# Optimization experiments

Hardware: AMD Instinct MI355X
Metric: run time of the kernel (lower is better)

Reference implementation:

```python
import jax, jax.numpy as jnp
import numpy as np

D_MODEL = 2048
EXP_RATE = 4
DEPTH = 1
EPS = 1e-5

def setup_inputs() -> dict:
    key = jax.random.key(0)
    k1, k2 = jax.random.split(key, 2)
    B, T, D, E = 4, 4096, D_MODEL, EXP_RATE
    x = jax.random.normal(k1, (B, T, D), dtype=jnp.float32)
    residual = jax.random.normal(k2, (B, T, D), dtype=jnp.float32)
    # static_alpha = cat([alpha0, eye(E)], dim=1) -> [E, E+1]
    alpha0 = np.zeros((E, 1), dtype=np.float32)
    alpha0[DEPTH % E, 0] = 1.0
    static_alpha = jnp.asarray(np.concatenate([alpha0, np.eye(E, dtype=np.float32)], axis=1))
    static_beta = jnp.ones((E,), dtype=jnp.float32)
    dynamic_alpha_fn = jnp.zeros((D, E + 1), dtype=jnp.float32)
    dynamic_alpha_scale = jnp.ones((1,), dtype=jnp.float32) * 0.01
    dynamic_beta_fn = jnp.zeros((D,), dtype=jnp.float32)
    dynamic_beta_scale = jnp.ones((1,), dtype=jnp.float32) * 0.01
    rms_weight = jnp.ones((D,), dtype=jnp.float32)
    return {
        "x": x, "residual": residual, "rms_weight": rms_weight,
        "static_alpha": static_alpha, "static_beta": static_beta,
        "dynamic_alpha_fn": dynamic_alpha_fn, "dynamic_alpha_scale": dynamic_alpha_scale,
        "dynamic_beta_fn": dynamic_beta_fn, "dynamic_beta_scale": dynamic_beta_scale,
    }

def reference(x, residual, rms_weight, static_alpha, static_beta,
              dynamic_alpha_fn, dynamic_alpha_scale, dynamic_beta_fn, dynamic_beta_scale):
    # RMSNorm (elementwise affine)
    norm_x = x * jax.lax.rsqrt(jnp.mean(x * x, axis=-1, keepdims=True) + EPS) * rms_weight
    # Dynamic params
    dyn_alpha = jnp.tanh(norm_x @ dynamic_alpha_fn) * dynamic_alpha_scale  # [B,T,E+1]
    dyn_beta = jnp.tanh(norm_x @ dynamic_beta_fn) * dynamic_beta_scale[0]  # [B,T]
    alpha = static_alpha[None, None] + dyn_alpha[:, :, None, :]  # [B,T,E,E+1]
    beta = static_beta[None, None] + dyn_beta[:, :, None]        # [B,T,E]
    # Width connection: einsum('btij,btjd->btid', alpha^T, x_expanded) with
    # x_expanded[b,t,j,:] == x[b,t,:] for all j  =>  mix_h[b,t,i,:] = (sum_j alpha[b,t,j,i]) * x[b,t,:]
    coeff = alpha.sum(axis=2)  # [B,T,E+1]
    # Depth connection: sum_e beta_e * residual + sum_{i>=1} mix_h_i  (dropout = identity at eval)
    out = residual * beta.sum(axis=-1, keepdims=True) + x * coeff[..., 1:].sum(axis=-1, keepdims=True)
    return out
```

## Files before the change

kernel.cpp:

```cpp
#include <hip/hip_runtime.h>


#define D_MODEL 2048
#define E_RATE 4
#define HC_EPS 1e-5f
#define NT 256
#define EPT 8

extern "C" __global__ void __launch_bounds__(NT)
hc_kernel(const float* __restrict__ x,
          const float* __restrict__ resid,
          const float* __restrict__ w,
          const float* __restrict__ sA,
          const float* __restrict__ sB,
          const float* __restrict__ fnA,
          const float* __restrict__ aScale,
          const float* __restrict__ fnB,
          const float* __restrict__ bScale,
          float* __restrict__ out)
{
    const int tid = threadIdx.x;
    const size_t rowBase = (size_t)blockIdx.x * D_MODEL;

    const float4* xr = (const float4*)(x + rowBase);
    float4 x0 = xr[2 * tid], x1 = xr[2 * tid + 1];
    float4 w0 = ((const float4*)w)[2 * tid];
    float4 w1 = ((const float4*)w)[2 * tid + 1];
    float4 b0 = ((const float4*)fnB)[2 * tid];
    float4 b1 = ((const float4*)fnB)[2 * tid + 1];

    float xf[EPT]  = {x0.x, x0.y, x0.z, x0.w, x1.x, x1.y, x1.z, x1.w};
    float wf[EPT]  = {w0.x, w0.y, w0.z, w0.w, w1.x, w1.y, w1.z, w1.w};
    float fbf[EPT] = {b0.x, b0.y, b0.z, b0.w, b1.x, b1.y, b1.z, b1.w};

    float xwp[EPT];
#pragma unroll
    for (int d = 0; d < EPT; d++) xwp[d] = xf[d] * wf[d];

    float vals[7];
#pragma unroll
    for (int j = 0; j < 7; j++) vals[j] = 0.0f;

#pragma unroll
    for (int d = 0; d < EPT; d++) {
        vals[6] += xf[d] * xf[d];
        vals[5] += xwp[d] * fbf[d];
    }

    const float4* fa4 = (const float4*)fnA;
#pragma unroll
    for (int j = 0; j < 10; j++) {
        float4 t4 = fa4[(size_t)tid * 10 + j];
        float fv[4] = {t4.x, t4.y, t4.z, t4.w};
#pragma unroll
        for (int q = 0; q < 4; q++) {
            const int e = j * 4 + q;
            const int d = e / 5;
            const int i = e % 5;
            vals[i] += xwp[d] * fv[q];
        }
    }

#pragma unroll
    for (int j = 0; j < 7; j++) {
        float v = vals[j];
        for (int off = 32; off > 0; off >>= 1) v += __shfl_xor(v, off, 64);
        vals[j] = v;
    }

    __shared__ float red[NT / 64][7];
    __shared__ float bc[2];
    const int wave = tid >> 6, lane = tid & 63;
    if (lane == 0) {
#pragma unroll
        for (int j = 0; j < 7; j++) red[wave][j] = vals[j];
    }
    __syncthreads();

    if (tid == 0) {
        float tot[7];
#pragma unroll
        for (int j = 0; j < 7; j++)
            tot[j] = red[0][j] + red[1][j] + red[2][j] + red[3][j];

        const float inv = rsqrtf(tot[6] * (1.0f / D_MODEL) + HC_EPS);
        const float asc = aScale[0];
        const float bsc = bScale[0];

        const float dynb = tanhf(tot[5] * inv) * bsc;
        float dyna_sum = 0.0f;
#pragma unroll
        for (int i = 1; i <= E_RATE; i++) dyna_sum += tanhf(tot[i] * inv) * asc;

        float SB = 0.0f;
#pragma unroll
        for (int e = 0; e < E_RATE; e++) SB += sB[e];
        float SA = 0.0f;
#pragma unroll
        for (int i = 1; i <= E_RATE; i++)
#pragma unroll
            for (int j = 0; j < E_RATE; j++) SA += sA[j * (E_RATE + 1) + i];

        bc[0] = SB + (float)E_RATE * dynb;
        bc[1] = SA + (float)E_RATE * dyna_sum;
    }
    __syncthreads();

    const float cR = bc[0], cX = bc[1];

    const float4* rr = (const float4*)(resid + rowBase);
    float4 r0 = rr[2 * tid], r1 = rr[2 * tid + 1];

    float4 o0, o1;
    o0.x = r0.x * cR + xf[0] * cX;
    o0.y = r0.y * cR + xf[1] * cX;
    o0.z = r0.z * cR + xf[2] * cX;
    o0.w = r0.w * cR + xf[3] * cX;
    o1.x = r1.x * cR + xf[4] * cX;
    o1.y = r1.y * cR + xf[5] * cX;
    o1.z = r1.z * cR + xf[6] * cX;
    o1.w = r1.w * cR + xf[7] * cX;

    float4* orow = (float4*)(out + rowBase);
    orow[2 * tid]     = o0;
    orow[2 * tid + 1] = o1;
}

extern "C" void kernel_launch(void* const* d_in, const int* in_sizes, int n_in,
                              void* d_out, int out_size, void* d_ws, size_t ws_size,
                              hipStream_t stream) {
    const float* x      = (const float*)d_in[0];
    const float* resid  = (const float*)d_in[1];
    const float* w      = (const float*)d_in[2];
    const float* sA     = (const float*)d_in[3];
    const float* sB     = (const float*)d_in[4];
    const float* fnA    = (const float*)d_in[5];
    const float* aScale = (const float*)d_in[6];
    const float* fnB    = (const float*)d_in[7];
    const float* bScale = (const float*)d_in[8];
    float* out          = (float*)d_out;

    const int n_tokens = in_sizes[0] / D_MODEL;

    hc_kernel<<<n_tokens, NT, 0, stream>>>(x, resid, w, sA, sB, fnA, aScale,
                                           fnB, bScale, out);
}
```

Baseline: 389.3 us.

## Process multiple tokens per block with prefetch and precomputed weight products

Each block now handles eight tokens, prefetching the next token's x and residual rows while reducing the current one. Products of the RMS weight with the dynamic alpha/beta projections are precomputed once per block and reused across tokens. The scalar coefficients are computed redundantly by every thread after a single barrier, with double-buffered shared reduction slots, and tanh uses a fast exp2/rcp approximation. This targets the per-block launch overhead, the two barriers and the exposed residual load latency, at the cost of more registers and slightly lower tanh precision.

```diff
diff --git a/kernel.cpp b/kernel.cpp
--- a/kernel.cpp
+++ b/kernel.cpp
@@ -6,8 +6,14 @@
 #define HC_EPS 1e-5f
 #define NT 256
 #define EPT 8
+#define TPB 8
 
-extern "C" __global__ void __launch_bounds__(NT)
+__device__ __forceinline__ float fast_tanh(float z) {
+    const float e = __builtin_amdgcn_exp2f(z * 2.8853900817779268f);
+    return fmaf(-2.0f, __builtin_amdgcn_rcpf(e + 1.0f), 1.0f);
+}
+
+extern "C" __global__ void __launch_bounds__(NT, 4)
 hc_kernel(const float* __restrict__ x,
           const float* __restrict__ resid,
           const float* __restrict__ w,
@@ -17,36 +23,27 @@
           const float* __restrict__ aScale,
           const float* __restrict__ fnB,
           const float* __restrict__ bScale,
-          float* __restrict__ out)
+          float* __restrict__ out,
+          const int n_tokens)
 {
-    const int tid = threadIdx.x;
-    const size_t rowBase = (size_t)blockIdx.x * D_MODEL;
+    const int tid  = threadIdx.x;
+    const int tok0 = blockIdx.x * TPB;
+    const int ntok = min(TPB, n_tokens - tok0);
+    const int wave = tid >> 6, lane = tid & 63;
 
-    const float4* xr = (const float4*)(x + rowBase);
-    float4 x0 = xr[2 * tid], x1 = xr[2 * tid + 1];
     float4 w0 = ((const float4*)w)[2 * tid];
     float4 w1 = ((const float4*)w)[2 * tid + 1];
     float4 b0 = ((const float4*)fnB)[2 * tid];
     float4 b1 = ((const float4*)fnB)[2 * tid + 1];
 
-    float xf[EPT]  = {x0.x, x0.y, x0.z, x0.w, x1.x, x1.y, x1.z, x1.w};
     float wf[EPT]  = {w0.x, w0.y, w0.z, w0.w, w1.x, w1.y, w1.z, w1.w};
     float fbf[EPT] = {b0.x, b0.y, b0.z, b0.w, b1.x, b1.y, b1.z, b1.w};
 
-    float xwp[EPT];
+    float wb[EPT];
 #pragma unroll
-    for (int d = 0; d < EPT; d++) xwp[d] = xf[d] * wf[d];
+    for (int d = 0; d < EPT; d++) wb[d] = wf[d] * fbf[d];
 
-    float vals[7];
-#pragma unroll
-    for (int j = 0; j < 7; j++) vals[j] = 0.0f;
-
-#pragma unroll
-    for (int d = 0; d < EPT; d++) {
-        vals[6] += xf[d] * xf[d];
-        vals[5] += xwp[d] * fbf[d];
-    }
-
+    float wa[EPT][E_RATE];
     const float4* fa4 = (const float4*)fnA;
 #pragma unroll
     for (int j = 0; j < 10; j++) {
@@ -57,73 +54,95 @@
             const int e = j * 4 + q;
             const int d = e / 5;
             const int i = e % 5;
-            vals[i] += xwp[d] * fv[q];
+            if (i >= 1) wa[d][i - 1] = fv[q] * wf[d];
         }
     }
 
+    const float SB = sB[0] + sB[1] + sB[2] + sB[3];
+    float SA = 0.0f;
 #pragma unroll
-    for (int j = 0; j < 7; j++) {
-        float v = vals[j];
-        for (int off = 32; off > 0; off >>= 1) v += __shfl_xor(v, off, 64);
-        vals[j] = v;
+    for (int i = 1; i <= E_RATE; i++)
+#pragma unroll
+        for (int j = 0; j < E_RATE; j++) SA += sA[j * (E_RATE + 1) + i];
+    const float asc = aScale[0];
+    const float bsc = bScale[0];
+
+    __shared__ float red[2][4][8];
+
+    const int F4 = D_MODEL / 4;
+    const float4* xr   = (const float4*)(x     + (size_t)tok0 * D_MODEL);
+    const float4* rr   = (const float4*)(resid + (size_t)tok0 * D_MODEL);
+    float4*       orow = (float4*)(out + (size_t)tok0 * D_MODEL);
+
+    float4 xn0 = xr[2 * tid], xn1 = xr[2 * tid + 1];
+    float4 rn0 = rr[2 * tid], rn1 = rr[2 * tid + 1];
+
+    for (int t = 0; t < ntok; ++t) {
+        const float4 x0 = xn0, x1 = xn1, r0 = rn0, r1 = rn1;
+        if (t + 1 < ntok) {
+            const int nb = (t + 1) * F4 + 2 * tid;
+            xn0 = xr[nb]; xn1 = xr[nb + 1];
+            rn0 = rr[nb]; rn1 = rr[nb + 1];
+        }
+
+        const float xf[EPT] = {x0.x, x0.y, x0.z, x0.w, x1.x, x1.y, x1.z, x1.w};
+
+        float vals[6] = {0.f, 0.f, 0.f, 0.f, 0.f, 0.f};
+#pragma unroll
+        for (int d = 0; d < EPT; d++) {
+            vals[5] = fmaf(xf[d], xf[d], vals[5]);
+            vals[4] = fmaf(xf[d], wb[d], vals[4]);
+            vals[0] = fmaf(xf[d], wa[d][0], vals[0]);
+            vals[1] = fmaf(xf[d], wa[d][1], vals[1]);
+            vals[2] = fmaf(xf[d], wa[d][2], vals[2]);
+            vals[3] = fmaf(xf[d], wa[d][3], vals[3]);
+        }
+
+#pragma unroll
+        for (int j = 0; j < 6; j++) {
+            float v = vals[j];
+#pragma unroll
+            for (int off = 32; off > 0; off >>= 1) v += __shfl_xor(v, off, 64);
+            vals[j] = v;
+        }
+
+        const int p = t & 1;
+        if (lane == 0) {
+#pragma unroll
+            for (int j = 0; j < 6; j++) red[p][wave][j] = vals[j];
+        }
+        asm volatile("s_waitcnt lgkmcnt(0)" ::: "memory");
+        __builtin_amdgcn_s_barrier();
+        asm volatile("" ::: "memory");
+
+        float tot[6];
+#pragma unroll
+        for (int j = 0; j < 6; j++)
+            tot[j] = (red[p][0][j] + red[p][1][j]) + (red[p][2][j] + red[p][3][j]);
+
+        const float inv  = rsqrtf(tot[5] * (1.0f / D_MODEL) + HC_EPS);
+        const float dynb = fast_tanh(tot[4] * inv) * bsc;
+        float dyna = 0.0f;
+#pragma unroll
+        for (int i = 0; i < E_RATE; i++) dyna += fast_tanh(tot[i] * inv);
+
+        const float cR = SB + (float)E_RATE * dynb;
+        const float cX = SA + (float)E_RATE * (dyna * asc);
+
+        float4 o0, o1;
+        o0.x = fmaf(r0.x, cR, x0.x * cX);
+        o0.y = fmaf(r0.y, cR, x0.y * cX);
+        o0.z = fmaf(r0.z, cR, x0.z * cX);
+        o0.w = fmaf(r0.w, cR, x0.w * cX);
+        o1.x = fmaf(r1.x, cR, x1.x * cX);
+        o1.y = fmaf(r1.y, cR, x1.y * cX);
+        o1.z = fmaf(r1.z, cR, x1.z * cX);
+        o1.w = fmaf(r1.w, cR, x1.w * cX);
+
+        const int ob = t * F4 + 2 * tid;
+        orow[ob]     = o0;
+        orow[ob + 1] = o1;
     }
-
-    __shared__ float red[NT / 64][7];
-    __shared__ float bc[2];
-    const int wave = tid >> 6, lane = tid & 63;
-    if (lane == 0) {
-#pragma unroll
-        for (int j = 0; j < 7; j++) red[wave][j] = vals[j];
-    }
-    __syncthreads();
-
-    if (tid == 0) {
-        float tot[7];
-#pragma unroll
-        for (int j = 0; j < 7; j++)
-            tot[j] = red[0][j] + red[1][j] + red[2][j] + red[3][j];
-
-        const float inv = rsqrtf(tot[6] * (1.0f / D_MODEL) + HC_EPS);
-        const float asc = aScale[0];
-        const float bsc = bScale[0];
-
-        const float dynb = tanhf(tot[5] * inv) * bsc;
-        float dyna_sum = 0.0f;
-#pragma unroll
-        for (int i = 1; i <= E_RATE; i++) dyna_sum += tanhf(tot[i] * inv) * asc;
-
-        float SB = 0.0f;
-#pragma unroll
-        for (int e = 0; e < E_RATE; e++) SB += sB[e];
-        float SA = 0.0f;
-#pragma unroll
-        for (int i = 1; i <= E_RATE; i++)
-#pragma unroll
-            for (int j = 0; j < E_RATE; j++) SA += sA[j * (E_RATE + 1) + i];
-
-        bc[0] = SB + (float)E_RATE * dynb;
-        bc[1] = SA + (float)E_RATE * dyna_sum;
-    }
-    __syncthreads();
-
-    const float cR = bc[0], cX = bc[1];
-
-    const float4* rr = (const float4*)(resid + rowBase);
-    float4 r0 = rr[2 * tid], r1 = rr[2 * tid + 1];
-
-    float4 o0, o1;
-    o0.x = r0.x * cR + xf[0] * cX;
-    o0.y = r0.y * cR + xf[1] * cX;
-    o0.z = r0.z * cR + xf[2] * cX;
-    o0.w = r0.w * cR + xf[3] * cX;
-    o1.x = r1.x * cR + xf[4] * cX;
-    o1.y = r1.y * cR + xf[5] * cX;
-    o1.z = r1.z * cR + xf[6] * cX;
-    o1.w = r1.w * cR + xf[7] * cX;
-
-    float4* orow = (float4*)(out + rowBase);
-    orow[2 * tid]     = o0;
-    orow[2 * tid + 1] = o1;
 }
 
 extern "C" void kernel_launch(void* const* d_in, const int* in_sizes, int n_in,
@@ -141,7 +160,8 @@
     float* out          = (float*)d_out;
 
     const int n_tokens = in_sizes[0] / D_MODEL;
+    const int grid = (n_tokens + TPB - 1) / TPB;
 
-    hc_kernel<<<n_tokens, NT, 0, stream>>>(x, resid, w, sA, sB, fnA, aScale,
-                                           fnB, bScale, out);
+    hc_kernel<<<grid, NT, 0, stream>>>(x, resid, w, sA, sB, fnA, aScale,
+                                       fnB, bScale, out, n_tokens);
 }
```

Result: faster. 328.2 us (-15.7%).
